# Performance work log

Hardware: AMD Instinct MI355X
Metric: run time of the kernel (lower is better)

## Reference

```python
import jax, jax.numpy as jnp
import numpy as np

N, B, D = 4, 256, 128  # agents, batch, latent dim; hidden = 2*D


def setup_inputs() -> dict:
    key = jax.random.key(0)
    k1, k2, k3, k4, k5 = jax.random.split(key, 5)
    z_all = jax.random.normal(k1, (N, B, D), dtype=jnp.float32)
    # per-agent MLP params, stacked over agents; torch Linear layout [out, in]
    W1 = jax.random.normal(k2, (N, 2 * D, D), dtype=jnp.float32) * 0.08
    b1 = jax.random.normal(k3, (N, 2 * D), dtype=jnp.float32) * 0.05
    W2 = jax.random.normal(k4, (N, 1, 2 * D), dtype=jnp.float32) * 0.06
    b2 = jax.random.normal(k5, (N, 1), dtype=jnp.float32) * 0.05
    return {"z_all": z_all, "W1": W1, "b1": b1, "W2": W2, "b2": b2}


def _value(z, W1i, b1i, W2i, b2i):
    # V_i(z): Linear(D,2D) -> tanh -> Linear(2D,1), squeezed to scalar
    h = jnp.tanh(W1i @ z + b1i)          # [2D]
    return jnp.dot(W2i[0], h) + b2i[0]   # scalar


def _pair_hessian(zb, W1i, b1i, W2i, b2i):
    # Hessian of V_i w.r.t. z, batched over B -> [B, D, D]
    hess = jax.hessian(lambda z: _value(z, W1i, b1i, W2i, b2i))
    return jax.vmap(hess)(zb)


def reference(z_all, W1, b1, W2, b2):
    Bn, Dn = z_all.shape[1], z_all.shape[2]
    zero = jnp.zeros((Bn, Dn, Dn), dtype=z_all.dtype)
    rows = []
    for i in range(N):
        cols = []
        for j in range(N):
            if i == j:
                cols.append(zero)
            else:
                cols.append(_pair_hessian(z_all[j], W1[i], b1[i], W2[i], b2[i]))
        rows.append(jnp.stack(cols, axis=0))
    return jnp.stack(rows, axis=0)  # [N, N, B, D, D]
```

## Files before the change

kernel.cpp:

```cpp
#include <hip/hip_runtime.h>
#include <hip/hip_bf16.h>

#define NA 4
#define BB 256
#define DDm 128
#define KKm 256

typedef __attribute__((ext_vector_type(4))) float f32x4;
typedef __attribute__((ext_vector_type(4))) unsigned int u32x4;
typedef __attribute__((ext_vector_type(8))) short bf16x8;

__device__ __forceinline__ unsigned int f2bf(float f) {
  unsigned int bits = __builtin_bit_cast(unsigned int, f);
  unsigned int lsb = (bits >> 16) & 1u;
  return (bits + 0x7fffu + lsb) >> 16;
}

__device__ __forceinline__ int swz_off(int a, int k2bytes) {
  return ((a << 9) + k2bytes) ^ ((a & 7) << 4);
}

__global__ __launch_bounds__(256) void prep_kernel(const float* __restrict__ W1,
                                                   unsigned short* __restrict__ Wt_g,
                                                   float* __restrict__ W1T) {
  int blk = blockIdx.x;
  int i = blk >> 3;
  int chunk = blk & 7;
  const float* W1i = W1 + i * KKm * DDm;
  char* Wti = (char*)(Wt_g + i * 32768);
  float* W1Ti = W1T + i * DDm * KKm;
  int base = chunk * 4096;
  for (int idx = base + threadIdx.x; idx < base + 4096; idx += 256) {
    int a = idx >> 8;
    int k = idx & 255;
    float v = W1i[k * DDm + a];
    W1Ti[a * KKm + k] = v;
    *(unsigned short*)(Wti + swz_off(a, k << 1)) = (unsigned short)f2bf(v);
  }
}

__global__ __launch_bounds__(256, 2) void hess_kernel(
    const float* __restrict__ z_all, const float* __restrict__ b1,
    const float* __restrict__ W2, const unsigned short* __restrict__ Wt_g,
    const float* __restrict__ W1T, float* __restrict__ out) {
  __shared__ __align__(16) unsigned short Wt[32768];
  __shared__ __align__(16) float s_lds[2][KKm];

  int t = threadIdx.x;
  int blk = blockIdx.x;
  int pair = blk >> 7;
  int bgrp = blk & 127;
  int i = pair >> 2;
  int j = pair & 3;

  if (i == j) {
    f32x4* zp = (f32x4*)(out + (((size_t)pair * BB + bgrp * 2) << 14));
    f32x4 z4 = (f32x4){0.f, 0.f, 0.f, 0.f};
#pragma unroll
    for (int q = 0; q < 32; ++q) zp[q * 256 + t] = z4;
    return;
  }

  {
    int wvi = t >> 6, lane = t & 63;
    const char* src = (const char*)(Wt_g + i * 32768);
#pragma unroll
    for (int it = 0; it < 16; ++it) {
      int off = (it * 4 + wvi) * 1024;
      __builtin_amdgcn_global_load_lds(
          (const __attribute__((address_space(1))) unsigned int*)(src + off + lane * 16),
          (__attribute__((address_space(3))) unsigned int*)((char*)Wt + off),
          16, 0, 0);
    }
  }

  {
    const float* w = W1T + i * DDm * KKm + t;
    const float* zj = z_all + ((size_t)j * BB + bgrp * 2) * DDm;
    float u0 = b1[i * KKm + t];
    float u1 = u0;
#pragma unroll 8
    for (int a = 0; a < DDm; ++a) {
      float wa = w[a * KKm];
      u0 = fmaf(wa, zj[a], u0);
      u1 = fmaf(wa, zj[DDm + a], u1);
    }
    float w2v = W2[i * KKm + t];
    float h0 = tanhf(u0), h1 = tanhf(u1);
    s_lds[0][t] = -2.0f * w2v * h0 * (1.0f - h0 * h0);
    s_lds[1][t] = -2.0f * w2v * h1 * (1.0f - h1 * h1);
  }
  __syncthreads();

  int wvi = t >> 6, lane = t & 63;
  int bl = wvi >> 1;
  int m0 = (wvi & 1) * 64;
  int g = lane >> 4;
  int lr = lane & 15;

  f32x4 acc[4][8];
#pragma unroll
  for (int mt = 0; mt < 4; ++mt)
#pragma unroll
    for (int nt = 0; nt < 8; ++nt) acc[mt][nt] = (f32x4){0.f, 0.f, 0.f, 0.f};

  for (int kc = 0; kc < 8; ++kc) {
    int kbyte = kc * 64 + g * 16;
    const f32x4* sp = (const f32x4*)&s_lds[bl][kc * 32 + g * 8];
    f32x4 sA = sp[0], sB = sp[1];
    float sv[8] = {sA[0], sA[1], sA[2], sA[3], sB[0], sB[1], sB[2], sB[3]};

    bf16x8 afr[4];
#pragma unroll
    for (int mt = 0; mt < 4; ++mt) {
      int row = m0 + mt * 16 + lr;
      u32x4 wq = *(const u32x4*)((const char*)Wt + swz_off(row, kbyte));
      u32x4 aq;
#pragma unroll
      for (int q = 0; q < 4; ++q) {
        float lo = __builtin_bit_cast(float, wq[q] << 16) * sv[2 * q];
        float hi = __builtin_bit_cast(float, wq[q] & 0xffff0000u) * sv[2 * q + 1];
        aq[q] = f2bf(lo) | (f2bf(hi) << 16);
      }
      afr[mt] = __builtin_bit_cast(bf16x8, aq);
    }

#pragma unroll
    for (int nt = 0; nt < 8; ++nt) {
      int row = nt * 16 + lr;
      bf16x8 bfr = __builtin_bit_cast(
          bf16x8, *(const u32x4*)((const char*)Wt + swz_off(row, kbyte)));
#pragma unroll
      for (int mt = 0; mt < 4; ++mt)
        acc[mt][nt] =
            __builtin_amdgcn_mfma_f32_16x16x32_bf16(afr[mt], bfr, acc[mt][nt], 0, 0, 0);
    }
  }

  int b = bgrp * 2 + bl;
  float* op = out + (((size_t)pair * BB + b) << 14);
#pragma unroll
  for (int mt = 0; mt < 4; ++mt) {
    int rbase = m0 + mt * 16 + g * 4;
#pragma unroll
    for (int nt = 0; nt < 8; ++nt) {
      int col = nt * 16 + lr;
#pragma unroll
      for (int q = 0; q < 4; ++q) op[(size_t)(rbase + q) * DDm + col] = acc[mt][nt][q];
    }
  }
}

extern "C" void kernel_launch(void* const* d_in, const int* in_sizes, int n_in,
                              void* d_out, int out_size, void* d_ws, size_t ws_size,
                              hipStream_t stream) {
  const float* z_all = (const float*)d_in[0];
  const float* W1 = (const float*)d_in[1];
  const float* b1 = (const float*)d_in[2];
  const float* W2 = (const float*)d_in[3];
  float* out = (float*)d_out;

  unsigned short* Wt_g = (unsigned short*)d_ws;
  float* W1T = (float*)((char*)d_ws + 262144);

  prep_kernel<<<32, 256, 0, stream>>>(W1, Wt_g, W1T);
  hess_kernel<<<16 * 128, 256, 0, stream>>>(z_all, b1, W2, Wt_g, W1T, out);
}
```

Baseline: 73.77 us.

## Process eight batch elements per block to amortize LDS weight staging

Each block now handles eight batch samples instead of two, so the 64KB bf16 W1 copy into LDS and the W1T read in the first layer are amortized over four times as many samples. Grid shrinks from 2048 to 512 blocks, and each wave loops over four samples in 32-row halves with smaller accumulator tiles. The bf16 rounding now uses the compiler's native conversion instead of a manual routine. Risk: 512 blocks give less parallelism on a large GPU and leave a longer serial loop per block, which may reduce latency hiding for the write-bound output.

```diff
diff --git a/kernel.cpp b/kernel.cpp
--- a/kernel.cpp
+++ b/kernel.cpp
@@ -44,29 +44,29 @@
     const float* __restrict__ W2, const unsigned short* __restrict__ Wt_g,
     const float* __restrict__ W1T, float* __restrict__ out) {
   __shared__ __align__(16) unsigned short Wt[32768];
-  __shared__ __align__(16) float s_lds[2][KKm];
+  __shared__ __align__(16) float s_lds[8][KKm];
 
   int t = threadIdx.x;
   int blk = blockIdx.x;
-  int pair = blk >> 7;
-  int bgrp = blk & 127;
+  int pair = blk >> 5;
+  int bgrp = blk & 31;
   int i = pair >> 2;
   int j = pair & 3;
 
   if (i == j) {
-    f32x4* zp = (f32x4*)(out + (((size_t)pair * BB + bgrp * 2) << 14));
+    f32x4* zp = (f32x4*)(out + (((size_t)pair * BB + bgrp * 8) << 14));
     f32x4 z4 = (f32x4){0.f, 0.f, 0.f, 0.f};
 #pragma unroll
-    for (int q = 0; q < 32; ++q) zp[q * 256 + t] = z4;
+    for (int q = 0; q < 128; ++q) zp[q * 256 + t] = z4;
     return;
   }
 
   {
-    int wvi = t >> 6, lane = t & 63;
+    int wv = t >> 6, lane = t & 63;
     const char* src = (const char*)(Wt_g + i * 32768);
 #pragma unroll
     for (int it = 0; it < 16; ++it) {
-      int off = (it * 4 + wvi) * 1024;
+      int off = (it * 4 + wv) * 1024;
       __builtin_amdgcn_global_load_lds(
           (const __attribute__((address_space(1))) unsigned int*)(src + off + lane * 16),
           (__attribute__((address_space(3))) unsigned int*)((char*)Wt + off),
@@ -76,78 +76,91 @@
 
   {
     const float* w = W1T + i * DDm * KKm + t;
-    const float* zj = z_all + ((size_t)j * BB + bgrp * 2) * DDm;
-    float u0 = b1[i * KKm + t];
-    float u1 = u0;
-#pragma unroll 8
+    const float* zj = z_all + ((size_t)j * BB + bgrp * 8) * DDm;
+    float ub = b1[i * KKm + t];
+    float u[8];
+#pragma unroll
+    for (int v = 0; v < 8; ++v) u[v] = ub;
+#pragma unroll 4
     for (int a = 0; a < DDm; ++a) {
       float wa = w[a * KKm];
-      u0 = fmaf(wa, zj[a], u0);
-      u1 = fmaf(wa, zj[DDm + a], u1);
+#pragma unroll
+      for (int v = 0; v < 8; ++v) u[v] = fmaf(wa, zj[v * DDm + a], u[v]);
     }
     float w2v = W2[i * KKm + t];
-    float h0 = tanhf(u0), h1 = tanhf(u1);
-    s_lds[0][t] = -2.0f * w2v * h0 * (1.0f - h0 * h0);
-    s_lds[1][t] = -2.0f * w2v * h1 * (1.0f - h1 * h1);
+#pragma unroll
+    for (int v = 0; v < 8; ++v) {
+      float h = tanhf(u[v]);
+      s_lds[v][t] = -2.0f * w2v * h * (1.0f - h * h);
+    }
   }
   __syncthreads();
 
   int wvi = t >> 6, lane = t & 63;
-  int bl = wvi >> 1;
-  int m0 = (wvi & 1) * 64;
   int g = lane >> 4;
   int lr = lane & 15;
+  int bset = wvi >> 1;
+  int rb0 = (wvi & 1) * 64;
 
-  f32x4 acc[4][8];
+  f32x4 accA[2][8], accB[2][8];
+
+  auto do_chunk = [&](f32x4 (&acc)[2][8], int rowbase, const float* sb, float* op) {
 #pragma unroll
-  for (int mt = 0; mt < 4; ++mt)
+    for (int mt = 0; mt < 2; ++mt)
 #pragma unroll
-    for (int nt = 0; nt < 8; ++nt) acc[mt][nt] = (f32x4){0.f, 0.f, 0.f, 0.f};
+      for (int nt = 0; nt < 8; ++nt) acc[mt][nt] = (f32x4){0.f, 0.f, 0.f, 0.f};
 
-  for (int kc = 0; kc < 8; ++kc) {
-    int kbyte = kc * 64 + g * 16;
-    const f32x4* sp = (const f32x4*)&s_lds[bl][kc * 32 + g * 8];
-    f32x4 sA = sp[0], sB = sp[1];
-    float sv[8] = {sA[0], sA[1], sA[2], sA[3], sB[0], sB[1], sB[2], sB[3]};
+    for (int kc = 0; kc < 8; ++kc) {
+      int kbyte = kc * 64 + g * 16;
+      const f32x4* sp = (const f32x4*)&sb[kc * 32 + g * 8];
+      f32x4 sA = sp[0], sB = sp[1];
+      float sv[8] = {sA[0], sA[1], sA[2], sA[3], sB[0], sB[1], sB[2], sB[3]};
 
-    bf16x8 afr[4];
+      bf16x8 afr[2];
 #pragma unroll
-    for (int mt = 0; mt < 4; ++mt) {
-      int row = m0 + mt * 16 + lr;
-      u32x4 wq = *(const u32x4*)((const char*)Wt + swz_off(row, kbyte));
-      u32x4 aq;
+      for (int mt = 0; mt < 2; ++mt) {
+        int row = rowbase + mt * 16 + lr;
+        u32x4 wq = *(const u32x4*)((const char*)Wt + swz_off(row, kbyte));
+        u32x4 aq;
 #pragma unroll
-      for (int q = 0; q < 4; ++q) {
-        float lo = __builtin_bit_cast(float, wq[q] << 16) * sv[2 * q];
-        float hi = __builtin_bit_cast(float, wq[q] & 0xffff0000u) * sv[2 * q + 1];
-        aq[q] = f2bf(lo) | (f2bf(hi) << 16);
+        for (int q = 0; q < 4; ++q) {
+          float lo = __builtin_bit_cast(float, wq[q] << 16) * sv[2 * q];
+          float hi = __builtin_bit_cast(float, wq[q] & 0xffff0000u) * sv[2 * q + 1];
+          unsigned int lb = __builtin_bit_cast(unsigned short, (__bf16)lo);
+          unsigned int hb = __builtin_bit_cast(unsigned short, (__bf16)hi);
+          aq[q] = lb | (hb << 16);
+        }
+        afr[mt] = __builtin_bit_cast(bf16x8, aq);
       }
-      afr[mt] = __builtin_bit_cast(bf16x8, aq);
+
+#pragma unroll
+      for (int nt = 0; nt < 8; ++nt) {
+        int row = nt * 16 + lr;
+        bf16x8 bfr = __builtin_bit_cast(
+            bf16x8, *(const u32x4*)((const char*)Wt + swz_off(row, kbyte)));
+        acc[0][nt] = __builtin_amdgcn_mfma_f32_16x16x32_bf16(afr[0], bfr, acc[0][nt], 0, 0, 0);
+        acc[1][nt] = __builtin_amdgcn_mfma_f32_16x16x32_bf16(afr[1], bfr, acc[1][nt], 0, 0, 0);
+      }
     }
 
 #pragma unroll
-    for (int nt = 0; nt < 8; ++nt) {
-      int row = nt * 16 + lr;
-      bf16x8 bfr = __builtin_bit_cast(
-          bf16x8, *(const u32x4*)((const char*)Wt + swz_off(row, kbyte)));
+    for (int mt = 0; mt < 2; ++mt) {
+      int rbase = rowbase + mt * 16 + g * 4;
 #pragma unroll
-      for (int mt = 0; mt < 4; ++mt)
-        acc[mt][nt] =
-            __builtin_amdgcn_mfma_f32_16x16x32_bf16(afr[mt], bfr, acc[mt][nt], 0, 0, 0);
+      for (int nt = 0; nt < 8; ++nt) {
+        int col = nt * 16 + lr;
+#pragma unroll
+        for (int q = 0; q < 4; ++q) op[(size_t)(rbase + q) * DDm + col] = acc[mt][nt][q];
+      }
     }
-  }
+  };
 
-  int b = bgrp * 2 + bl;
-  float* op = out + (((size_t)pair * BB + b) << 14);
-#pragma unroll
-  for (int mt = 0; mt < 4; ++mt) {
-    int rbase = m0 + mt * 16 + g * 4;
-#pragma unroll
-    for (int nt = 0; nt < 8; ++nt) {
-      int col = nt * 16 + lr;
-#pragma unroll
-      for (int q = 0; q < 4; ++q) op[(size_t)(rbase + q) * DDm + col] = acc[mt][nt][q];
-    }
+  for (int bb = 0; bb < 4; ++bb) {
+    int bloc = bset * 4 + bb;
+    const float* sb = &s_lds[bloc][0];
+    float* op = out + (((size_t)pair * BB + bgrp * 8 + bloc) << 14);
+    do_chunk(accA, rb0, sb, op);
+    do_chunk(accB, rb0 + 32, sb, op);
   }
 }
 
@@ -164,5 +177,5 @@
   float* W1T = (float*)((char*)d_ws + 262144);
 
   prep_kernel<<<32, 256, 0, stream>>>(W1, Wt_g, W1T);
-  hess_kernel<<<16 * 128, 256, 0, stream>>>(z_all, b1, W2, Wt_g, W1T, out);
+  hess_kernel<<<16 * 32, 256, 0, stream>>>(z_all, b1, W2, Wt_g, W1T, out);
 }
```

After: 69.12 us. -6.3%, faster.
